# Kernel tuning notes

Measured on AMD Instinct MI355X. Metric: run time of the kernel, lower is better.

Reference implementation:

```python
import jax, jax.numpy as jnp
import numpy as np

PERIOD = 0.1


def setup_inputs() -> dict:
    key = jax.random.key(0)
    ks = jax.random.split(key, 16)
    B, N, C, P = 2, 3072, 4, 4
    E, H, T, F, L = 512, 8, 256, 64, 4
    Nt = N // P

    def rn(k, shape, scale=0.02):
        return jax.random.normal(k, shape, jnp.float32) * scale

    return {
        "x": jax.random.normal(ks[0], (B, N, C), jnp.float32),
        "t": jax.random.normal(ks[1], (B, T), jnp.float32),
        "vec_map": jax.random.normal(ks[2], (B, N, 3), jnp.float32),
        # RelativeBias dense: freq features -> heads
        "W_rb": rn(ks[3], (F, H)),
        "b_rb": jnp.zeros((H,), jnp.float32),
        # patch embedding dense: P*C -> E
        "W_embed": rn(ks[4], (P * C, E), 0.1),
        "b_embed": jnp.zeros((E,), jnp.float32),
        "pos_emb": rn(ks[5], (Nt, E)),
        # stacked per-block params (leading dim L = n_blocks)
        "ada1_W1": rn(ks[6], (L, T, T)),
        "ada1_b1": jnp.zeros((L, T), jnp.float32),
        "ada1_W2": rn(ks[7], (L, T, 3 * E)),
        "ada1_b2": jnp.zeros((L, 3 * E), jnp.float32),
        "qkv_W": rn(ks[8], (L, E, 3 * E)),
        "qkv_b": jnp.zeros((L, 3 * E), jnp.float32),
        "out_W": rn(ks[9], (L, E, E)),
        "out_b": jnp.zeros((L, E), jnp.float32),
        "ada2_W1": rn(ks[10], (L, T, T)),
        "ada2_b1": jnp.zeros((L, T), jnp.float32),
        "ada2_W2": rn(ks[11], (L, T, 3 * E)),
        "ada2_b2": jnp.zeros((L, 3 * E), jnp.float32),
        "mlp_W1": rn(ks[12], (L, E, 4 * E)),
        "mlp_b1": jnp.zeros((L, 4 * E), jnp.float32),
        "mlp_W2": rn(ks[13], (L, 4 * E, E)),
        "mlp_b2": jnp.zeros((L, E), jnp.float32),
    }


def _layernorm(y):
    # flax LayerNorm(use_bias=False, use_scale=False), eps=1e-6
    mu = jnp.mean(y, axis=-1, keepdims=True)
    var = jnp.mean(jnp.square(y - mu), axis=-1, keepdims=True)
    return (y - mu) * jax.lax.rsqrt(var + 1e-6)


def _adaln(t, W1, b1, W2, b2):
    h = jax.nn.silu(t @ W1 + b1)
    m = (h @ W2 + b2)[..., None, :]  # (B, 1, 3E)
    return jnp.split(m, 3, axis=-1)


def reference(x, t, vec_map, W_rb, b_rb, W_embed, b_embed, pos_emb,
              ada1_W1, ada1_b1, ada1_W2, ada1_b2, qkv_W, qkv_b, out_W, out_b,
              ada2_W1, ada2_b1, ada2_W2, ada2_b2, mlp_W1, mlp_b1, mlp_W2, mlp_b2):
    B, N, C = x.shape
    Nt, E = pos_emb.shape
    P = N // Nt
    F, H = W_rb.shape
    hd = E // H

    # patchify tokens: (B, N, C) -> (B, Nt, P*C); mean vec per patch
    xp = x.reshape(B, Nt, P * C)
    vp = vec_map.reshape(B, Nt, P, 3).mean(axis=-2)

    # relative bias logits (B, Nt, Nt, H)
    v = vp / jnp.linalg.norm(vp, axis=-1, keepdims=True)
    dif = v[..., :, None, :] - v[..., None, :, :]
    dot = 1.0 - 0.5 * jnp.sum(dif * dif, axis=-1)
    angle = jnp.arccos(jnp.clip(dot, -1.0, 1.0)) / 0.005
    freqs = jnp.linspace(0, 1, F // 2) / PERIOD
    ph = freqs * angle[..., None]  # (B, Nt, Nt, F/2)
    pos = jnp.concatenate((jnp.sin(ph), jnp.cos(ph)), axis=-1)
    bias = pos @ W_rb + b_rb

    # patch embed + learned positional embedding
    h0 = xp @ W_embed + b_embed + pos_emb
    inv_sqrt_hd = 1.0 / jnp.sqrt(jnp.float32(hd))

    def block(xc, params):
        (aW1, ab1, aW2, ab2, qW, qb, oW, ob,
         cW1, cb1, cW2, cb2, mW1, mb1, mW2, mb2) = params
        g1, be1, al1 = _adaln(t, aW1, ab1, aW2, ab2)
        y = (g1 + 1.0) * _layernorm(xc) + be1
        qkv = (y @ qW + qb).reshape(B, Nt, H, 3, hd)
        q, k, vv = qkv[..., 0, :], qkv[..., 1, :], qkv[..., 2, :]
        logits = jnp.einsum('bqht,bkht->bqkh', q, k) * inv_sqrt_hd + bias
        logits = logits - jnp.max(logits, axis=-2, keepdims=True)
        attn = jax.nn.softmax(logits, axis=-2)  # softmax over keys (K axis)
        y = jnp.einsum('bqkh,bkht->bqht', attn, vv).reshape(B, Nt, E)
        y = y @ oW + ob
        xc = xc + al1 * y / jnp.sqrt(1.0 + al1 * al1)
        g2, be2, al2 = _adaln(t, cW1, cb1, cW2, cb2)
        y = (g2 + 1.0) * _layernorm(xc) + be2
        y = jax.nn.gelu(y @ mW1 + mb1) @ mW2 + mb2
        xc = xc + al2 * y / jnp.sqrt(1.0 + al2 * al2)
        return xc, None

    params = (ada1_W1, ada1_b1, ada1_W2, ada1_b2, qkv_W, qkv_b, out_W, out_b,
              ada2_W1, ada2_b1, ada2_W2, ada2_b2, mlp_W1, mlp_b1, mlp_W2, mlp_b2)
    out, _ = jax.lax.scan(block, h0, params)
    return out
```

## Files before the change

### kernel.cpp

```cpp
#include <hip/hip_runtime.h>
#include <hip/hip_bf16.h>


#define NT 768
#define EDIM 512
#define E3 1536
#define E4 2048
#define NH 8
#define TB 2

typedef unsigned short ushort_t;
typedef __attribute__((ext_vector_type(8))) short bf16x8;
typedef __attribute__((ext_vector_type(4))) float f32x4;

#define GLOAD(src, dst) __builtin_amdgcn_global_load_lds( \
    (const __attribute__((address_space(1))) unsigned int*)(src), \
    (__attribute__((address_space(3))) unsigned int*)(dst), 16, 0, 0)

__device__ inline float b2f(ushort_t u) {
    unsigned int i = ((unsigned int)u) << 16; float f;
    __builtin_memcpy(&f, &i, 4); return f;
}
__device__ inline ushort_t f2b(float f) {
    __hip_bfloat16 h = __float2bfloat16(f);
    ushort_t u; __builtin_memcpy(&u, &h, 2); return u;
}
__device__ inline float gelu_tanh(float u) {
    float z = 1.5957691216057308f * (u + 0.044715f * u * u * u);
    z = fminf(z, 40.f);
    float t = __expf(z);
    float th = (t - 1.f) / (t + 1.f);
    return 0.5f * u * (1.f + th);
}

__global__ __launch_bounds__(256) void k_vnorm(const float* __restrict__ vm, float* __restrict__ v) {
    int idx = blockIdx.x * 256 + threadIdx.x;
    if (idx >= TB * NT) return;
    float s0 = 0.f, s1 = 0.f, s2 = 0.f;
    #pragma unroll
    for (int p = 0; p < 4; ++p) {
        s0 += vm[(idx * 4 + p) * 3 + 0];
        s1 += vm[(idx * 4 + p) * 3 + 1];
        s2 += vm[(idx * 4 + p) * 3 + 2];
    }
    float inv = 1.f / sqrtf(s0 * s0 + s1 * s1 + s2 * s2);
    v[idx * 3 + 0] = s0 * inv; v[idx * 3 + 1] = s1 * inv; v[idx * 3 + 2] = s2 * inv;
}

__global__ __launch_bounds__(256) void k_bias(const float* __restrict__ v, const float* __restrict__ W_rb,
                                              const float* __restrict__ b_rb, ushort_t* __restrict__ biasT) {
    int bq = blockIdx.x; int b = bq / NT, q = bq % NT;
    __shared__ float sv[NT * 3];
    int tid = threadIdx.x, lane = tid & 63, wave = tid >> 6;
    for (int i = tid; i < NT * 3; i += 256) sv[i] = v[b * NT * 3 + i];

    int g = lane >> 4, col = lane & 15;
    ushort_t tw[16];
    #pragma unroll
    for (int j = 0; j < 8; ++j) {
        float wsv = (col < 8) ? W_rb[(g * 8 + j) * 8 + col] : 0.f;
        float wcv = (col < 8) ? W_rb[(32 + g * 8 + j) * 8 + col] : 0.f;
        tw[j] = f2b(wsv); tw[8 + j] = f2b(wcv);
    }
    bf16x8 bsf, bcf;
    __builtin_memcpy(&bsf, tw, 16);
    __builtin_memcpy(&bcf, tw + 8, 16);
    float brh = (col < 8) ? b_rb[col] : 0.f;
    __syncthreads();

    float vq0 = sv[q * 3], vq1 = sv[q * 3 + 1], vq2 = sv[q * 3 + 2];
    float gf = (float)(8 * g);

    for (int it = 0; it < 12; ++it) {
        int tile = (it * 4 + wave) * 16;
        int p = tile + col;
        float d0 = vq0 - sv[p * 3], d1 = vq1 - sv[p * 3 + 1], d2 = vq2 - sv[p * 3 + 2];
        float dot = 1.f - 0.5f * (d0 * d0 + d1 * d1 + d2 * d2);
        dot = fminf(1.f, fmaxf(-1.f, dot));
        float theta = acosf(dot) * (2000.f / 31.f);
        float s1, c1; __sincosf(theta, &s1, &c1);
        float sg, cg; __sincosf(theta * gf, &sg, &cg);
        ushort_t fs[16];
        #pragma unroll
        for (int j = 0; j < 8; ++j) {
            fs[j] = f2b(sg); fs[8 + j] = f2b(cg);
            float ns = sg * c1 + cg * s1;
            cg = cg * c1 - sg * s1;
            sg = ns;
        }
        bf16x8 asf, acf;
        __builtin_memcpy(&asf, fs, 16);
        __builtin_memcpy(&acf, fs + 8, 16);
        f32x4 acc = {0.f, 0.f, 0.f, 0.f};
        acc = __builtin_amdgcn_mfma_f32_16x16x32_bf16(asf, bsf, acc, 0, 0, 0);
        acc = __builtin_amdgcn_mfma_f32_16x16x32_bf16(acf, bcf, acc, 0, 0, 0);
        if (col < 8) {
            ushort_t o[4];
            #pragma unroll
            for (int r = 0; r < 4; ++r) o[r] = f2b(acc[r] + brh);
            long off = (long)(b * 8 + col) * NT * NT + (long)q * NT + tile + 4 * g;
            uint2 pk;
            pk.x = (unsigned int)o[0] | ((unsigned int)o[1] << 16);
            pk.y = (unsigned int)o[2] | ((unsigned int)o[3] << 16);
            *(uint2*)(biasT + off) = pk;
        }
    }
}

__global__ __launch_bounds__(256) void k_embed(const float* __restrict__ x, const float* __restrict__ W,
                                               const float* __restrict__ be, const float* __restrict__ pe,
                                               float* __restrict__ xc) {
    int row = blockIdx.x; int nt = row % NT;
    __shared__ float sx[16];
    int tid = threadIdx.x;
    if (tid < 16) sx[tid] = x[row * 16 + tid];
    __syncthreads();
    for (int e = tid; e < EDIM; e += 256) {
        float a = be[e] + pe[nt * EDIM + e];
        #pragma unroll
        for (int j = 0; j < 16; ++j) a += sx[j] * W[j * EDIM + e];
        xc[(long)row * EDIM + e] = a;
    }
}

__global__ __launch_bounds__(256) void k_adaln(const float* __restrict__ t,
    const float* __restrict__ a1W1, const float* __restrict__ a1b1, const float* __restrict__ a1W2, const float* __restrict__ a1b2,
    const float* __restrict__ a2W1, const float* __restrict__ a2b1, const float* __restrict__ a2W2, const float* __restrict__ a2b2,
    float* __restrict__ ada) {
    int blk = blockIdx.x; int b = blk & 1, lw = blk >> 1; int which = lw & 1, l = lw >> 1;
    const float* W1 = (which ? a2W1 : a1W1) + (long)l * 256 * 256;
    const float* b1 = (which ? a2b1 : a1b1) + l * 256;
    const float* W2 = (which ? a2W2 : a1W2) + (long)l * 256 * E3;
    const float* b2 = (which ? a2b2 : a1b2) + l * E3;
    __shared__ float st[256], sh[256];
    int tid = threadIdx.x;
    st[tid] = t[b * 256 + tid];
    __syncthreads();
    float a = b1[tid];
    for (int i = 0; i < 256; ++i) a += st[i] * W1[i * 256 + tid];
    sh[tid] = a / (1.f + __expf(-a));
    __syncthreads();
    int c = blockIdx.y * 256 + tid;
    float m = b2[c];
    for (int i = 0; i < 256; ++i) m += sh[i] * W2[i * E3 + c];
    ada[(long)(lw * 2 + b) * E3 + c] = m;
}

__global__ __launch_bounds__(256) void k_lnmod(const float* __restrict__ xc, const float* __restrict__ ada,
                                               ushort_t* __restrict__ out, int lw) {
    int row = blockIdx.x; int b = row / NT;
    const float* ap = ada + (long)(lw * 2 + b) * E3;
    int tid = threadIdx.x;
    float2 vv = *(const float2*)(xc + (long)row * EDIM + tid * 2);
    float s1 = vv.x + vv.y, s2 = vv.x * vv.x + vv.y * vv.y;
    for (int o = 32; o; o >>= 1) { s1 += __shfl_down(s1, o); s2 += __shfl_down(s2, o); }
    __shared__ float sr[8];
    if ((tid & 63) == 0) { sr[tid >> 6] = s1; sr[4 + (tid >> 6)] = s2; }
    __syncthreads();
    s1 = sr[0] + sr[1] + sr[2] + sr[3];
    s2 = sr[4] + sr[5] + sr[6] + sr[7];
    float mu = s1 * (1.f / 512.f);
    float var = s2 * (1.f / 512.f) - mu * mu;
    float inv = rsqrtf(var + 1e-6f);
    int e = tid * 2;
    float r0 = (ap[e] + 1.f) * ((vv.x - mu) * inv) + ap[512 + e];
    float r1 = (ap[e + 1] + 1.f) * ((vv.y - mu) * inv) + ap[512 + e + 1];
    unsigned int pk = (unsigned int)f2b(r0) | ((unsigned int)f2b(r1) << 16);
    ((unsigned int*)out)[(long)row * 256 + tid] = pk;
}

__global__ __launch_bounds__(256) void k_wT(const float* __restrict__ W, ushort_t* __restrict__ Wt,
                                            int Kd, int Nd) {
    const float* Wp = W + (long)blockIdx.z * Kd * Nd;
    ushort_t* Wtp = Wt + (long)blockIdx.z * Kd * Nd;
    int n0 = blockIdx.x * 64, k0 = blockIdx.y * 64;
    __shared__ float s[64][65];
    int tid = threadIdx.x;
    #pragma unroll
    for (int it = 0; it < 4; ++it) {
        int idx = tid + it * 256;
        int r = idx >> 4, c4 = (idx & 15) * 4;
        float4 vv = *(const float4*)(Wp + (long)(k0 + r) * Nd + n0 + c4);
        s[r][c4] = vv.x; s[r][c4 + 1] = vv.y; s[r][c4 + 2] = vv.z; s[r][c4 + 3] = vv.w;
    }
    __syncthreads();
    #pragma unroll
    for (int it = 0; it < 4; ++it) {
        int idx = tid + it * 256;
        int rn = idx >> 4, ck = (idx & 15) * 4;
        long base = (long)(n0 + rn) * Kd + k0 + ck;
        #pragma unroll
        for (int j = 0; j < 4; ++j) Wtp[base + j] = f2b(s[ck + j][rn]);
    }
}

__global__ __launch_bounds__(256) void k_vT(const ushort_t* __restrict__ qkv16, ushort_t* __restrict__ vT) {
    int bh = blockIdx.y; int b = bh >> 3, h = bh & 7;
    int nt0 = blockIdx.x * 64;
    __shared__ ushort_t s[64][80];
    int tid = threadIdx.x;
    #pragma unroll
    for (int it = 0; it < 2; ++it) {
        int idx = tid + it * 256;
        int rnt = idx >> 3, c8 = (idx & 7) * 8;
        bf16x8 vv = *(const bf16x8*)(qkv16 + ((long)(b * NT + nt0 + rnt) * E3 + h * 192 + 128 + c8));
        *(bf16x8*)&s[rnt][c8] = vv;
    }
    __syncthreads();
    #pragma unroll
    for (int it = 0; it < 2; ++it) {
        int idx = tid + it * 256;
        int d = idx >> 3, n8 = (idx & 7) * 8;
        ushort_t tmp[8];
        #pragma unroll
        for (int j = 0; j < 8; ++j) tmp[j] = s[n8 + j][d];
        bf16x8 ov; __builtin_memcpy(&ov, tmp, 16);
        *(bf16x8*)(vT + ((long)bh * 64 + d) * NT + nt0 + n8) = ov;
    }
}

__global__ __launch_bounds__(256) void k_attn(const ushort_t* __restrict__ qkv16,
        const ushort_t* __restrict__ vT, const ushort_t* __restrict__ biasT,
        ushort_t* __restrict__ attnb) {
    int qt = blockIdx.x, bh = blockIdx.y;
    int b = bh >> 3, h = bh & 7;
    __shared__ __align__(16) ushort_t Ks[4096];
    __shared__ __align__(16) ushort_t Vs[4096];
    __shared__ __align__(16) ushort_t Bi[4096];
    int tid = threadIdx.x, lane = tid & 63, wave = tid >> 6;
    int g = lane >> 4, c = lane & 15;
    int ls = lane & 7, lr = lane >> 3;
    int stg_col = (ls ^ lr) * 8;
    int q0 = qt * 64;

    bf16x8 aq[2];
    {
        const ushort_t* qp = qkv16 + ((long)(b * NT + q0 + wave * 16 + c) * E3) + h * 192;
        aq[0] = *(const bf16x8*)(qp + g * 8);
        aq[1] = *(const bf16x8*)(qp + 32 + g * 8);
    }
    float m_r[4], l_r[4];
    f32x4 o_acc[4];
    #pragma unroll
    for (int rr = 0; rr < 4; ++rr) { m_r[rr] = -1e30f; l_r[rr] = 0.f; }
    #pragma unroll
    for (int nf = 0; nf < 4; ++nf) o_acc[nf] = f32x4{0.f, 0.f, 0.f, 0.f};

    for (int kt = 0; kt < 12; ++kt) {
        int k0 = kt * 64;
        #pragma unroll
        for (int is = 0; is < 2; ++is) {
            int row = is * 32 + wave * 8 + lr;
            int dstb = (is * 32 + wave * 8) * 64;
            GLOAD(qkv16 + (long)(b * NT + k0 + row) * E3 + h * 192 + 64 + stg_col, Ks + dstb);
            GLOAD(vT + ((long)bh * 64 + row) * NT + k0 + stg_col, Vs + dstb);
            GLOAD(biasT + (long)bh * NT * NT + (long)(q0 + row) * NT + k0 + ls * 8, Bi + dstb);
        }
        __syncthreads();
        f32x4 s[4];
        #pragma unroll
        for (int nf = 0; nf < 4; ++nf) {
            s[nf] = f32x4{0.f, 0.f, 0.f, 0.f};
            #pragma unroll
            for (int kh = 0; kh < 2; ++kh) {
                int row = nf * 16 + c;
                bf16x8 bk = *(const bf16x8*)(Ks + row * 64 + (((kh * 4 + g) ^ (row & 7))) * 8);
                s[nf] = __builtin_amdgcn_mfma_f32_16x16x32_bf16(aq[kh], bk, s[nf], 0, 0, 0);
            }
        }
        float p[4][4], mt[4];
        #pragma unroll
        for (int rr = 0; rr < 4; ++rr) {
            int ql = wave * 16 + g * 4 + rr;
            #pragma unroll
            for (int nf = 0; nf < 4; ++nf)
                p[nf][rr] = s[nf][rr] * 0.125f + b2f(Bi[ql * 64 + nf * 16 + c]);
            float mx = fmaxf(fmaxf(p[0][rr], p[1][rr]), fmaxf(p[2][rr], p[3][rr]));
            mx = fmaxf(mx, __shfl_xor(mx, 1));
            mx = fmaxf(mx, __shfl_xor(mx, 2));
            mx = fmaxf(mx, __shfl_xor(mx, 4));
            mx = fmaxf(mx, __shfl_xor(mx, 8));
            mt[rr] = mx;
        }
        #pragma unroll
        for (int rr = 0; rr < 4; ++rr) {
            float mnew = fmaxf(m_r[rr], mt[rr]);
            float sc = __expf(m_r[rr] - mnew);
            m_r[rr] = mnew;
            float rsum = 0.f;
            #pragma unroll
            for (int nf = 0; nf < 4; ++nf) {
                p[nf][rr] = __expf(p[nf][rr] - mnew);
                rsum += p[nf][rr];
            }
            rsum += __shfl_xor(rsum, 1); rsum += __shfl_xor(rsum, 2);
            rsum += __shfl_xor(rsum, 4); rsum += __shfl_xor(rsum, 8);
            l_r[rr] = l_r[rr] * sc + rsum;
            #pragma unroll
            for (int nf = 0; nf < 4; ++nf) o_acc[nf][rr] *= sc;
        }
        #pragma unroll
        for (int nf = 0; nf < 4; ++nf) {
            int kl = nf * 16 + c;
            int slot = kl >> 3, win = kl & 7;
            #pragma unroll
            for (int rr = 0; rr < 4; ++rr) {
                int ql = wave * 16 + g * 4 + rr;
                Bi[ql * 64 + ((slot ^ (ql & 7)) * 8) + win] = f2b(p[nf][rr]);
            }
        }
        asm volatile("s_waitcnt lgkmcnt(0)" ::: "memory");
        bf16x8 ap[2];
        #pragma unroll
        for (int kh = 0; kh < 2; ++kh) {
            int ql = wave * 16 + c;
            ap[kh] = *(const bf16x8*)(Bi + ql * 64 + (((kh * 4 + g) ^ (ql & 7))) * 8);
        }
        #pragma unroll
        for (int nf = 0; nf < 4; ++nf) {
            #pragma unroll
            for (int kh = 0; kh < 2; ++kh) {
                int row = nf * 16 + c;
                bf16x8 bv = *(const bf16x8*)(Vs + row * 64 + (((kh * 4 + g) ^ (row & 7))) * 8);
                o_acc[nf] = __builtin_amdgcn_mfma_f32_16x16x32_bf16(ap[kh], bv, o_acc[nf], 0, 0, 0);
            }
        }
        __syncthreads();
    }
    #pragma unroll
    for (int nf = 0; nf < 4; ++nf) {
        #pragma unroll
        for (int rr = 0; rr < 4; ++rr) {
            int ql = wave * 16 + g * 4 + rr;
            Ks[ql * 64 + nf * 16 + c] = f2b(o_acc[nf][rr] / l_r[rr]);
        }
    }
    asm volatile("s_waitcnt lgkmcnt(0)" ::: "memory");
    __syncthreads();
    int orow = wave * 16 + (lane >> 2);
    int ocol = (lane & 3) * 16;
    const ushort_t* srcO = Ks + orow * 64 + ocol;
    ushort_t* dstO = attnb + (long)(b * NT + q0 + orow) * EDIM + h * 64 + ocol;
    *(bf16x8*)(dstO) = *(const bf16x8*)(srcO);
    *(bf16x8*)(dstO + 8) = *(const bf16x8*)(srcO + 8);
}

template<int EPI>
__global__ __launch_bounds__(256) void k_mm64(
        const ushort_t* __restrict__ A0, const ushort_t* __restrict__ B0,
        const float* __restrict__ bias, const float* __restrict__ xin,
        const float* __restrict__ ada, int lw, void* __restrict__ C0,
        int K, int lda, int ldb, int ldc) {
    __shared__ __align__(16) ushort_t As[2][4096];
    __shared__ __align__(16) ushort_t Bs[2][4096];
    int tid = threadIdx.x, lane = tid & 63, wave = tid >> 6;
    int wm = wave >> 1, wn = wave & 1;
    int m0 = blockIdx.y * 64, n0 = blockIdx.x * 64;
    int lr = lane >> 3, ls = lane & 7;
    int stg_col = (ls ^ lr) * 8;
    int r = lane & 15, g = lane >> 4, rs = r & 7;
    int nt = K >> 6;

    f32x4 acc[2][2];
    #pragma unroll
    for (int i = 0; i < 2; ++i)
        #pragma unroll
        for (int j = 0; j < 2; ++j) acc[i][j] = f32x4{0.f, 0.f, 0.f, 0.f};

#define STAGE64(buf, t) { \
        int k0_ = (t) * 64; \
        _Pragma("unroll") \
        for (int c0 = 0; c0 < 4; ++c0) { \
            int ch = wave * 4 + c0; \
            if (ch < 8) { \
                GLOAD(A0 + (long)(m0 + ch * 8 + lr) * lda + k0_ + stg_col, &As[buf][ch * 512]); \
            } else { \
                GLOAD(B0 + (long)(n0 + (ch - 8) * 8 + lr) * ldb + k0_ + stg_col, &Bs[buf][(ch - 8) * 512]); \
            } \
        } }

    STAGE64(0, 0);
    __syncthreads();
    int cur = 0;
    for (int t = 0; t < nt; ++t) {
        if (t + 1 < nt) STAGE64(cur ^ 1, t + 1);
        bf16x8 af[2][2], bf[2][2];
        #pragma unroll
        for (int i = 0; i < 2; ++i) {
            int row = wm * 32 + i * 16 + r;
            #pragma unroll
            for (int kh = 0; kh < 2; ++kh)
                af[i][kh] = *(const bf16x8*)(&As[cur][row * 64 + (((kh * 4 + g) ^ rs)) * 8]);
        }
        #pragma unroll
        for (int j = 0; j < 2; ++j) {
            int row = wn * 32 + j * 16 + r;
            #pragma unroll
            for (int kh = 0; kh < 2; ++kh)
                bf[j][kh] = *(const bf16x8*)(&Bs[cur][row * 64 + (((kh * 4 + g) ^ rs)) * 8]);
        }
        #pragma unroll
        for (int kh = 0; kh < 2; ++kh)
            #pragma unroll
            for (int i = 0; i < 2; ++i)
                #pragma unroll
                for (int j = 0; j < 2; ++j)
                    acc[i][j] = __builtin_amdgcn_mfma_f32_16x16x32_bf16(af[i][kh], bf[j][kh], acc[i][j], 0, 0, 0);
        __syncthreads();
        cur ^= 1;
    }
#undef STAGE64

    int gr4 = g * 4, cL = lane & 15;
    if constexpr (EPI == 0 || EPI == 1) {
        ushort_t* C = (ushort_t*)C0;
        #pragma unroll
        for (int i = 0; i < 2; ++i) {
            int mrow = m0 + wm * 32 + i * 16 + gr4;
            #pragma unroll
            for (int j = 0; j < 2; ++j) {
                int n = n0 + wn * 32 + j * 16 + cL;
                float bn = bias[n];
                #pragma unroll
                for (int rr = 0; rr < 4; ++rr) {
                    float vv = acc[i][j][rr] + bn;
                    if constexpr (EPI == 1) vv = gelu_tanh(vv);
                    C[(long)(mrow + rr) * ldc + n] = f2b(vv);
                }
            }
        }
    } else {
        float* C = (float*)C0;
        #pragma unroll
        for (int i = 0; i < 2; ++i) {
            int mrow = m0 + wm * 32 + i * 16 + gr4;
            int bb = (mrow >= NT) ? 1 : 0;
            const float* al = ada + (long)(lw * 2 + bb) * E3 + 1024;
            #pragma unroll
            for (int j = 0; j < 2; ++j) {
                int n = n0 + wn * 32 + j * 16 + cL;
                float a = al[n];
                float sc = a * rsqrtf(1.f + a * a);
                float bn = bias[n];
                #pragma unroll
                for (int rr = 0; rr < 4; ++rr) {
                    long idx = (long)(mrow + rr) * ldc + n;
                    C[idx] = xin[idx] + sc * (acc[i][j][rr] + bn);
                }
            }
        }
    }
}

extern "C" void kernel_launch(void* const* d_in, const int* in_sizes, int n_in,
                              void* d_out, int out_size, void* d_ws, size_t ws_size,
                              hipStream_t stream) {
    const float* x       = (const float*)d_in[0];
    const float* t       = (const float*)d_in[1];
    const float* vec_map = (const float*)d_in[2];
    const float* W_rb    = (const float*)d_in[3];
    const float* b_rb    = (const float*)d_in[4];
    const float* W_embed = (const float*)d_in[5];
    const float* b_embed = (const float*)d_in[6];
    const float* pos_emb = (const float*)d_in[7];
    const float* a1W1    = (const float*)d_in[8];
    const float* a1b1    = (const float*)d_in[9];
    const float* a1W2    = (const float*)d_in[10];
    const float* a1b2    = (const float*)d_in[11];
    const float* qkv_W   = (const float*)d_in[12];
    const float* qkv_b   = (const float*)d_in[13];
    const float* out_W   = (const float*)d_in[14];
    const float* out_b   = (const float*)d_in[15];
    const float* a2W1    = (const float*)d_in[16];
    const float* a2b1    = (const float*)d_in[17];
    const float* a2W2    = (const float*)d_in[18];
    const float* a2b2    = (const float*)d_in[19];
    const float* mlp_W1  = (const float*)d_in[20];
    const float* mlp_b1  = (const float*)d_in[21];
    const float* mlp_W2  = (const float*)d_in[22];
    const float* mlp_b2  = (const float*)d_in[23];

    float* ws = (float*)d_ws;
    size_t o = 0;
    float* v        = ws + o; o += 8192;
    ushort_t* biasT = (ushort_t*)(ws + o); o += 4718592;
    float* ada      = ws + o; o += 24576;
    float* xc       = ws + o; o += 786432;
    ushort_t* ln16  = (ushort_t*)(ws + o); o += 393216;
    ushort_t* qkv16 = (ushort_t*)(ws + o); o += 1179648;
    ushort_t* vT    = (ushort_t*)(ws + o); o += 393216;
    ushort_t* attnb = (ushort_t*)(ws + o); o += 393216;
    ushort_t* mlph  = (ushort_t*)(ws + o); o += 1572864;
    ushort_t* qkvWt = (ushort_t*)(ws + o); o += 1572864;
    ushort_t* outWt = (ushort_t*)(ws + o); o += 524288;
    ushort_t* mlp1Wt = (ushort_t*)(ws + o); o += 2097152;
    ushort_t* mlp2Wt = (ushort_t*)(ws + o); o += 2097152;

    k_vnorm<<<6, 256, 0, stream>>>(vec_map, v);
    k_bias<<<TB * NT, 256, 0, stream>>>(v, W_rb, b_rb, biasT);
    k_embed<<<TB * NT, 256, 0, stream>>>(x, W_embed, b_embed, pos_emb, xc);
    k_adaln<<<dim3(16, 6), 256, 0, stream>>>(t, a1W1, a1b1, a1W2, a1b2, a2W1, a2b1, a2W2, a2b2, ada);
    k_wT<<<dim3(24, 8, 4), 256, 0, stream>>>(qkv_W,  qkvWt,  512, 1536);
    k_wT<<<dim3(8,  8, 4), 256, 0, stream>>>(out_W,  outWt,  512, 512);
    k_wT<<<dim3(32, 8, 4), 256, 0, stream>>>(mlp_W1, mlp1Wt, 512, 2048);
    k_wT<<<dim3(8, 32, 4), 256, 0, stream>>>(mlp_W2, mlp2Wt, 2048, 512);

    for (int l = 0; l < 4; ++l) {
        int lw0 = l * 2, lw1 = l * 2 + 1;
        k_lnmod<<<TB * NT, 256, 0, stream>>>(xc, ada, ln16, lw0);
        k_mm64<0><<<dim3(24, 24), 256, 0, stream>>>(
            ln16, qkvWt + (long)l * 786432, qkv_b + l * E3, nullptr, nullptr, 0,
            qkv16, 512, 512, 512, E3);
        k_vT<<<dim3(12, 16), 256, 0, stream>>>(qkv16, vT);
        k_attn<<<dim3(12, 16), 256, 0, stream>>>(qkv16, vT, biasT, attnb);
        k_mm64<5><<<dim3(8, 24), 256, 0, stream>>>(
            attnb, outWt + (long)l * 262144, out_b + l * EDIM, xc, ada, lw0,
            xc, 512, 512, 512, EDIM);
        k_lnmod<<<TB * NT, 256, 0, stream>>>(xc, ada, ln16, lw1);
        k_mm64<1><<<dim3(32, 24), 256, 0, stream>>>(
            ln16, mlp1Wt + (long)l * 1048576, mlp_b1 + l * E4, nullptr, nullptr, 0,
            mlph, 512, 512, 512, E4);
        k_mm64<5><<<dim3(8, 24), 256, 0, stream>>>(
            mlph, mlp2Wt + (long)l * 1048576, mlp_b2 + l * EDIM, xc, ada, lw1,
            (l == 3) ? (float*)d_out : xc, 2048, 2048, 2048, EDIM);
    }
}
```

Before: 411.7 us.

## Fuse vnorm into bias, merge weight transposes, fuse V transpose, double-buffer attention

Computes the normalized patch vectors inside k_bias, which removes the k_vnorm launch and its buffer. The four weight-transpose launches become one k_wTall launch. The V transpose moves into the QKV GEMM epilogue, so the separate k_vT kernel and one launch per layer disappear. The attention kernel double-buffers its K/V/bias LDS tiles so the next tile's loads overlap compute. The costs are doubled LDS use in attention, which may lower occupancy, and scattered 8-byte stores for vT in the GEMM epilogue.

```diff
diff --git a/kernel.cpp b/kernel.cpp
--- a/kernel.cpp
+++ b/kernel.cpp
@@ -33,26 +33,19 @@
     return 0.5f * u * (1.f + th);
 }
 
-__global__ __launch_bounds__(256) void k_vnorm(const float* __restrict__ vm, float* __restrict__ v) {
-    int idx = blockIdx.x * 256 + threadIdx.x;
-    if (idx >= TB * NT) return;
-    float s0 = 0.f, s1 = 0.f, s2 = 0.f;
-    #pragma unroll
-    for (int p = 0; p < 4; ++p) {
-        s0 += vm[(idx * 4 + p) * 3 + 0];
-        s1 += vm[(idx * 4 + p) * 3 + 1];
-        s2 += vm[(idx * 4 + p) * 3 + 2];
-    }
-    float inv = 1.f / sqrtf(s0 * s0 + s1 * s1 + s2 * s2);
-    v[idx * 3 + 0] = s0 * inv; v[idx * 3 + 1] = s1 * inv; v[idx * 3 + 2] = s2 * inv;
-}
-
-__global__ __launch_bounds__(256) void k_bias(const float* __restrict__ v, const float* __restrict__ W_rb,
+__global__ __launch_bounds__(256) void k_bias(const float* __restrict__ vm, const float* __restrict__ W_rb,
                                               const float* __restrict__ b_rb, ushort_t* __restrict__ biasT) {
     int bq = blockIdx.x; int b = bq / NT, q = bq % NT;
     __shared__ float sv[NT * 3];
     int tid = threadIdx.x, lane = tid & 63, wave = tid >> 6;
-    for (int i = tid; i < NT * 3; i += 256) sv[i] = v[b * NT * 3 + i];
+    for (int i = tid; i < NT; i += 256) {
+        const float* vp = vm + ((long)b * 3072 + i * 4) * 3;
+        float s0 = vp[0] + vp[3] + vp[6] + vp[9];
+        float s1 = vp[1] + vp[4] + vp[7] + vp[10];
+        float s2 = vp[2] + vp[5] + vp[8] + vp[11];
+        float inv = rsqrtf(s0 * s0 + s1 * s1 + s2 * s2);
+        sv[i * 3 + 0] = s0 * inv; sv[i * 3 + 1] = s1 * inv; sv[i * 3 + 2] = s2 * inv;
+    }
 
     int g = lane >> 4, col = lane & 15;
     ushort_t tw[16];
@@ -169,53 +162,37 @@
     ((unsigned int*)out)[(long)row * 256 + tid] = pk;
 }
 
-__global__ __launch_bounds__(256) void k_wT(const float* __restrict__ W, ushort_t* __restrict__ Wt,
-                                            int Kd, int Nd) {
-    const float* Wp = W + (long)blockIdx.z * Kd * Nd;
-    ushort_t* Wtp = Wt + (long)blockIdx.z * Kd * Nd;
-    int n0 = blockIdx.x * 64, k0 = blockIdx.y * 64;
+__global__ __launch_bounds__(256) void k_wTall(
+        const float* __restrict__ qkvW, const float* __restrict__ outW,
+        const float* __restrict__ m1W, const float* __restrict__ m2W,
+        ushort_t* __restrict__ qkvWt, ushort_t* __restrict__ outWt,
+        ushort_t* __restrict__ m1Wt, ushort_t* __restrict__ m2Wt) {
+    int idx = blockIdx.x, l = blockIdx.y;
+    const float* W; ushort_t* Wt; int Kd, Nd, ntile, ktile;
+    if (idx < 192)      { W = qkvW; Wt = qkvWt; Kd = 512;  Nd = 1536; ntile = idx % 24; ktile = idx / 24; }
+    else if (idx < 256) { W = outW; Wt = outWt; Kd = 512;  Nd = 512;  idx -= 192; ntile = idx % 8;  ktile = idx / 8; }
+    else if (idx < 512) { W = m1W;  Wt = m1Wt;  Kd = 512;  Nd = 2048; idx -= 256; ntile = idx % 32; ktile = idx / 32; }
+    else                { W = m2W;  Wt = m2Wt;  Kd = 2048; Nd = 512;  idx -= 512; ntile = idx % 8;  ktile = idx / 8; }
+    const float* Wp = W + (long)l * Kd * Nd;
+    ushort_t* Wtp = Wt + (long)l * Kd * Nd;
+    int n0 = ntile * 64, k0 = ktile * 64;
     __shared__ float s[64][65];
     int tid = threadIdx.x;
     #pragma unroll
     for (int it = 0; it < 4; ++it) {
-        int idx = tid + it * 256;
-        int r = idx >> 4, c4 = (idx & 15) * 4;
+        int i2 = tid + it * 256;
+        int r = i2 >> 4, c4 = (i2 & 15) * 4;
         float4 vv = *(const float4*)(Wp + (long)(k0 + r) * Nd + n0 + c4);
         s[r][c4] = vv.x; s[r][c4 + 1] = vv.y; s[r][c4 + 2] = vv.z; s[r][c4 + 3] = vv.w;
     }
     __syncthreads();
     #pragma unroll
     for (int it = 0; it < 4; ++it) {
-        int idx = tid + it * 256;
-        int rn = idx >> 4, ck = (idx & 15) * 4;
+        int i2 = tid + it * 256;
+        int rn = i2 >> 4, ck = (i2 & 15) * 4;
         long base = (long)(n0 + rn) * Kd + k0 + ck;
         #pragma unroll
         for (int j = 0; j < 4; ++j) Wtp[base + j] = f2b(s[ck + j][rn]);
-    }
-}
-
-__global__ __launch_bounds__(256) void k_vT(const ushort_t* __restrict__ qkv16, ushort_t* __restrict__ vT) {
-    int bh = blockIdx.y; int b = bh >> 3, h = bh & 7;
-    int nt0 = blockIdx.x * 64;
-    __shared__ ushort_t s[64][80];
-    int tid = threadIdx.x;
-    #pragma unroll
-    for (int it = 0; it < 2; ++it) {
-        int idx = tid + it * 256;
-        int rnt = idx >> 3, c8 = (idx & 7) * 8;
-        bf16x8 vv = *(const bf16x8*)(qkv16 + ((long)(b * NT + nt0 + rnt) * E3 + h * 192 + 128 + c8));
-        *(bf16x8*)&s[rnt][c8] = vv;
-    }
-    __syncthreads();
-    #pragma unroll
-    for (int it = 0; it < 2; ++it) {
-        int idx = tid + it * 256;
-        int d = idx >> 3, n8 = (idx & 7) * 8;
-        ushort_t tmp[8];
-        #pragma unroll
-        for (int j = 0; j < 8; ++j) tmp[j] = s[n8 + j][d];
-        bf16x8 ov; __builtin_memcpy(&ov, tmp, 16);
-        *(bf16x8*)(vT + ((long)bh * 64 + d) * NT + nt0 + n8) = ov;
     }
 }
 
@@ -224,9 +201,9 @@
         ushort_t* __restrict__ attnb) {
     int qt = blockIdx.x, bh = blockIdx.y;
     int b = bh >> 3, h = bh & 7;
-    __shared__ __align__(16) ushort_t Ks[4096];
-    __shared__ __align__(16) ushort_t Vs[4096];
-    __shared__ __align__(16) ushort_t Bi[4096];
+    __shared__ __align__(16) ushort_t Ks[2][4096];
+    __shared__ __align__(16) ushort_t Vs[2][4096];
+    __shared__ __align__(16) ushort_t Bi[2][4096];
     int tid = threadIdx.x, lane = tid & 63, wave = tid >> 6;
     int g = lane >> 4, c = lane & 15;
     int ls = lane & 7, lr = lane >> 3;
@@ -246,17 +223,22 @@
     #pragma unroll
     for (int nf = 0; nf < 4; ++nf) o_acc[nf] = f32x4{0.f, 0.f, 0.f, 0.f};
 
+#define STAGEA(buf, kt) { \
+        int k0_ = (kt) * 64; \
+        _Pragma("unroll") \
+        for (int is = 0; is < 2; ++is) { \
+            int row = is * 32 + wave * 8 + lr; \
+            int dstb = (is * 32 + wave * 8) * 64; \
+            GLOAD(qkv16 + (long)(b * NT + k0_ + row) * E3 + h * 192 + 64 + stg_col, &Ks[buf][dstb]); \
+            GLOAD(vT + ((long)bh * 64 + row) * NT + k0_ + stg_col, &Vs[buf][dstb]); \
+            GLOAD(biasT + (long)bh * NT * NT + (long)(q0 + row) * NT + k0_ + ls * 8, &Bi[buf][dstb]); \
+        } }
+
+    STAGEA(0, 0);
+    __syncthreads();
+    int cur = 0;
     for (int kt = 0; kt < 12; ++kt) {
-        int k0 = kt * 64;
-        #pragma unroll
-        for (int is = 0; is < 2; ++is) {
-            int row = is * 32 + wave * 8 + lr;
-            int dstb = (is * 32 + wave * 8) * 64;
-            GLOAD(qkv16 + (long)(b * NT + k0 + row) * E3 + h * 192 + 64 + stg_col, Ks + dstb);
-            GLOAD(vT + ((long)bh * 64 + row) * NT + k0 + stg_col, Vs + dstb);
-            GLOAD(biasT + (long)bh * NT * NT + (long)(q0 + row) * NT + k0 + ls * 8, Bi + dstb);
-        }
-        __syncthreads();
+        if (kt + 1 < 12) STAGEA(cur ^ 1, kt + 1);
         f32x4 s[4];
         #pragma unroll
         for (int nf = 0; nf < 4; ++nf) {
@@ -264,7 +246,7 @@
             #pragma unroll
             for (int kh = 0; kh < 2; ++kh) {
                 int row = nf * 16 + c;
-                bf16x8 bk = *(const bf16x8*)(Ks + row * 64 + (((kh * 4 + g) ^ (row & 7))) * 8);
+                bf16x8 bk = *(const bf16x8*)(&Ks[cur][row * 64 + (((kh * 4 + g) ^ (row & 7))) * 8]);
                 s[nf] = __builtin_amdgcn_mfma_f32_16x16x32_bf16(aq[kh], bk, s[nf], 0, 0, 0);
             }
         }
@@ -274,7 +256,7 @@
             int ql = wave * 16 + g * 4 + rr;
             #pragma unroll
             for (int nf = 0; nf < 4; ++nf)
-                p[nf][rr] = s[nf][rr] * 0.125f + b2f(Bi[ql * 64 + nf * 16 + c]);
+                p[nf][rr] = s[nf][rr] * 0.125f + b2f(Bi[cur][ql * 64 + nf * 16 + c]);
             float mx = fmaxf(fmaxf(p[0][rr], p[1][rr]), fmaxf(p[2][rr], p[3][rr]));
             mx = fmaxf(mx, __shfl_xor(mx, 1));
             mx = fmaxf(mx, __shfl_xor(mx, 2));
@@ -306,7 +288,7 @@
             #pragma unroll
             for (int rr = 0; rr < 4; ++rr) {
                 int ql = wave * 16 + g * 4 + rr;
-                Bi[ql * 64 + ((slot ^ (ql & 7)) * 8) + win] = f2b(p[nf][rr]);
+                Bi[cur][ql * 64 + ((slot ^ (ql & 7)) * 8) + win] = f2b(p[nf][rr]);
             }
         }
         asm volatile("s_waitcnt lgkmcnt(0)" ::: "memory");
@@ -314,32 +296,34 @@
         #pragma unroll
         for (int kh = 0; kh < 2; ++kh) {
             int ql = wave * 16 + c;
-            ap[kh] = *(const bf16x8*)(Bi + ql * 64 + (((kh * 4 + g) ^ (ql & 7))) * 8);
+            ap[kh] = *(const bf16x8*)(&Bi[cur][ql * 64 + (((kh * 4 + g) ^ (ql & 7))) * 8]);
         }
         #pragma unroll
         for (int nf = 0; nf < 4; ++nf) {
             #pragma unroll
             for (int kh = 0; kh < 2; ++kh) {
                 int row = nf * 16 + c;
-                bf16x8 bv = *(const bf16x8*)(Vs + row * 64 + (((kh * 4 + g) ^ (row & 7))) * 8);
+                bf16x8 bv = *(const bf16x8*)(&Vs[cur][row * 64 + (((kh * 4 + g) ^ (row & 7))) * 8]);
                 o_acc[nf] = __builtin_amdgcn_mfma_f32_16x16x32_bf16(ap[kh], bv, o_acc[nf], 0, 0, 0);
             }
         }
         __syncthreads();
-    }
+        cur ^= 1;
+    }
+#undef STAGEA
     #pragma unroll
     for (int nf = 0; nf < 4; ++nf) {
         #pragma unroll
         for (int rr = 0; rr < 4; ++rr) {
             int ql = wave * 16 + g * 4 + rr;
-            Ks[ql * 64 + nf * 16 + c] = f2b(o_acc[nf][rr] / l_r[rr]);
+            Ks[0][ql * 64 + nf * 16 + c] = f2b(o_acc[nf][rr] / l_r[rr]);
         }
     }
     asm volatile("s_waitcnt lgkmcnt(0)" ::: "memory");
     __syncthreads();
     int orow = wave * 16 + (lane >> 2);
     int ocol = (lane & 3) * 16;
-    const ushort_t* srcO = Ks + orow * 64 + ocol;
+    const ushort_t* srcO = &Ks[0][orow * 64 + ocol];
     ushort_t* dstO = attnb + (long)(b * NT + q0 + orow) * EDIM + h * 64 + ocol;
     *(bf16x8*)(dstO) = *(const bf16x8*)(srcO);
     *(bf16x8*)(dstO + 8) = *(const bf16x8*)(srcO + 8);
@@ -350,7 +334,7 @@
         const ushort_t* __restrict__ A0, const ushort_t* __restrict__ B0,
         const float* __restrict__ bias, const float* __restrict__ xin,
         const float* __restrict__ ada, int lw, void* __restrict__ C0,
-        int K, int lda, int ldb, int ldc) {
+        int K, int lda, int ldb, int ldc, ushort_t* __restrict__ vTout) {
     __shared__ __align__(16) ushort_t As[2][4096];
     __shared__ __align__(16) ushort_t Bs[2][4096];
     int tid = threadIdx.x, lane = tid & 63, wave = tid >> 6;
@@ -384,7 +368,7 @@
     int cur = 0;
     for (int t = 0; t < nt; ++t) {
         if (t + 1 < nt) STAGE64(cur ^ 1, t + 1);
-        bf16x8 af[2][2], bf[2][2];
+        bf16x8 af[2][2], bfr[2][2];
         #pragma unroll
         for (int i = 0; i < 2; ++i) {
             int row = wm * 32 + i * 16 + r;
@@ -397,7 +381,7 @@
             int row = wn * 32 + j * 16 + r;
             #pragma unroll
             for (int kh = 0; kh < 2; ++kh)
-                bf[j][kh] = *(const bf16x8*)(&Bs[cur][row * 64 + (((kh * 4 + g) ^ rs)) * 8]);
+                bfr[j][kh] = *(const bf16x8*)(&Bs[cur][row * 64 + (((kh * 4 + g) ^ rs)) * 8]);
         }
         #pragma unroll
         for (int kh = 0; kh < 2; ++kh)
@@ -405,7 +389,7 @@
             for (int i = 0; i < 2; ++i)
                 #pragma unroll
                 for (int j = 0; j < 2; ++j)
-                    acc[i][j] = __builtin_amdgcn_mfma_f32_16x16x32_bf16(af[i][kh], bf[j][kh], acc[i][j], 0, 0, 0);
+                    acc[i][j] = __builtin_amdgcn_mfma_f32_16x16x32_bf16(af[i][kh], bfr[j][kh], acc[i][j], 0, 0, 0);
         __syncthreads();
         cur ^= 1;
     }
@@ -421,11 +405,27 @@
             for (int j = 0; j < 2; ++j) {
                 int n = n0 + wn * 32 + j * 16 + cL;
                 float bn = bias[n];
+                ushort_t o[4];
                 #pragma unroll
                 for (int rr = 0; rr < 4; ++rr) {
                     float vv = acc[i][j][rr] + bn;
                     if constexpr (EPI == 1) vv = gelu_tanh(vv);
-                    C[(long)(mrow + rr) * ldc + n] = f2b(vv);
+                    o[rr] = f2b(vv);
+                    C[(long)(mrow + rr) * ldc + n] = o[rr];
+                }
+                if constexpr (EPI == 0) {
+                    if (vTout) {
+                        int seg = n % 192;
+                        if (seg >= 128) {
+                            int h = n / 192, d = seg - 128;
+                            int b2 = (mrow >= NT) ? 1 : 0;
+                            int tok = mrow - b2 * NT;
+                            uint2 pk;
+                            pk.x = (unsigned int)o[0] | ((unsigned int)o[1] << 16);
+                            pk.y = (unsigned int)o[2] | ((unsigned int)o[3] << 16);
+                            *(uint2*)(vTout + ((long)((b2 * 8 + h) * 64 + d)) * NT + tok) = pk;
+                        }
+                    }
                 }
             }
         }
@@ -482,7 +482,6 @@
 
     float* ws = (float*)d_ws;
     size_t o = 0;
-    float* v        = ws + o; o += 8192;
     ushort_t* biasT = (ushort_t*)(ws + o); o += 4718592;
     float* ada      = ws + o; o += 24576;
     float* xc       = ws + o; o += 786432;
@@ -496,32 +495,28 @@
     ushort_t* mlp1Wt = (ushort_t*)(ws + o); o += 2097152;
     ushort_t* mlp2Wt = (ushort_t*)(ws + o); o += 2097152;
 
-    k_vnorm<<<6, 256, 0, stream>>>(vec_map, v);
-    k_bias<<<TB * NT, 256, 0, stream>>>(v, W_rb, b_rb, biasT);
+    k_bias<<<TB * NT, 256, 0, stream>>>(vec_map, W_rb, b_rb, biasT);
     k_embed<<<TB * NT, 256, 0, stream>>>(x, W_embed, b_embed, pos_emb, xc);
     k_adaln<<<dim3(16, 6), 256, 0, stream>>>(t, a1W1, a1b1, a1W2, a1b2, a2W1, a2b1, a2W2, a2b2, ada);
-    k_wT<<<dim3(24, 8, 4), 256, 0, stream>>>(qkv_W,  qkvWt,  512, 1536);
-    k_wT<<<dim3(8,  8, 4), 256, 0, stream>>>(out_W,  outWt,  512, 512);
-    k_wT<<<dim3(32, 8, 4), 256, 0, stream>>>(mlp_W1, mlp1Wt, 512, 2048);
-    k_wT<<<dim3(8, 32, 4), 256, 0, stream>>>(mlp_W2, mlp2Wt, 2048, 512);
+    k_wTall<<<dim3(768, 4), 256, 0, stream>>>(qkv_W, out_W, mlp_W1, mlp_W2,
+                                              qkvWt, outWt, mlp1Wt, mlp2Wt);
 
     for (int l = 0; l < 4; ++l) {
         int lw0 = l * 2, lw1 = l * 2 + 1;
         k_lnmod<<<TB * NT, 256, 0, stream>>>(xc, ada, ln16, lw0);
         k_mm64<0><<<dim3(24, 24), 256, 0, stream>>>(
             ln16, qkvWt + (long)l * 786432, qkv_b + l * E3, nullptr, nullptr, 0,
-            qkv16, 512, 512, 512, E3);
-        k_vT<<<dim3(12, 16), 256, 0, stream>>>(qkv16, vT);
+            qkv16, 512, 512, 512, E3, vT);
         k_attn<<<dim3(12, 16), 256, 0, stream>>>(qkv16, vT, biasT, attnb);
         k_mm64<5><<<dim3(8, 24), 256, 0, stream>>>(
             attnb, outWt + (long)l * 262144, out_b + l * EDIM, xc, ada, lw0,
-            xc, 512, 512, 512, EDIM);
+            xc, 512, 512, 512, EDIM, nullptr);
         k_lnmod<<<TB * NT, 256, 0, stream>>>(xc, ada, ln16, lw1);
         k_mm64<1><<<dim3(32, 24), 256, 0, stream>>>(
             ln16, mlp1Wt + (long)l * 1048576, mlp_b1 + l * E4, nullptr, nullptr, 0,
-            mlph, 512, 512, 512, E4);
+            mlph, 512, 512, 512, E4, nullptr);
         k_mm64<5><<<dim3(8, 24), 256, 0, stream>>>(
             mlph, mlp2Wt + (long)l * 1048576, mlp_b2 + l * EDIM, xc, ada, lw1,
-            (l == 3) ? (float*)d_out : xc, 2048, 2048, 2048, EDIM);
-    }
-}
+            (l == 3) ? (float*)d_out : xc, 2048, 2048, 2048, EDIM, nullptr);
+    }
+}
```

Result: faster. 395.4 us (-4.0%).
